# Kernel optimization log

Hardware: AMD Instinct MI355X
Metric: run time of the kernel (lower is better)

Reference implementation:

```python
import jax, jax.numpy as jnp
import numpy as np

B, L, D, H = 65536, 20, 4, 1024
T = 61  # output_length; 60 RK4 steps


def setup_inputs() -> dict:
    key = jax.random.key(0)
    ks = jax.random.split(key, 16)
    # small positive states so the quadratic SEIR dynamics stay finite over 60 steps
    xx = jax.random.uniform(ks[0], (B, L, D), dtype=jnp.float32) * 0.1
    dims = [L * D] + [H] * 6 + [3]
    inp = {"xx": xx}
    for i in range(7):
        scale = 1.0 / np.sqrt(dims[i])
        W = jax.random.normal(ks[1 + 2 * i], (dims[i], dims[i + 1]), dtype=jnp.float32) * scale
        if i == 6:
            W = W * 1e-3  # keep beta/gamma/sigma small -> stable integration
        inp[f"W{i}"] = W
        inp[f"b{i}"] = jnp.zeros((dims[i + 1],), jnp.float32)
    inp["output_length"] = T
    return inp


def reference(xx, W0, b0, W1, b1, W2, b2, W3, b3, W4, b4, W5, b5, W6, b6, output_length):
    h = xx.reshape(xx.shape[0], -1)  # (B, L*D)
    for W, b in ((W0, b0), (W1, b1), (W2, b2), (W3, b3), (W4, b4), (W5, b5)):
        h = jax.nn.leaky_relu(h @ W + b, negative_slope=0.01)
    out = h @ W6 + b6  # (B, 3)
    beta, gamma, sigma = out[:, 0:1], out[:, 1:2], out[:, 2:3]  # each (B,1)

    initial = xx[:, 0]  # (B, 4) = S,E,I,R at t0
    S0, E0, I0, R0 = (initial[:, i:i + 1] for i in range(4))
    # self.step = 1 in the torch module, so dt is folded in as 1.0

    def derivs(S, E, I):
        SI = beta * S * I
        return -SI, SI - sigma * E, sigma * E - gamma * I, gamma * I

    def body(carry, _):
        S, E, I, R = carry
        k1S, k1E, k1I, k1R = derivs(S, E, I)
        k2S, k2E, k2I, k2R = derivs(S + 0.5 * k1S, E + 0.5 * k1E, I + 0.5 * k1I)
        k3S, k3E, k3I, k3R = derivs(S + 0.5 * k2S, E + 0.5 * k2E, I + 0.5 * k2I)
        k4S, k4E, k4I, k4R = derivs(S + k3S, E + k3E, I + k3I)
        upd = lambda f, k1, k2, k3, k4: f + (k1 + 2 * k2 + 2 * k3 + k4) / 6.0
        new = (upd(S, k1S, k2S, k3S, k4S),
               upd(E, k1E, k2E, k3E, k4E),
               upd(I, k1I, k2I, k3I, k4I),
               upd(R, k1R, k2R, k3R, k4R))
        return new, jnp.concatenate(new, axis=1)  # (B,4) per step

    _, ys = jax.lax.scan(body, (S0, E0, I0, R0), None, length=output_length - 1)
    y0 = jnp.concatenate([S0, E0, I0, R0], axis=1)  # (B,4)
    y = jnp.concatenate([y0[None], ys], axis=0)     # (T,B,4)
    return jnp.transpose(y, (1, 0, 2))              # (B,T,4) in S,E,I,R order
```

## Files before the change

### kernel.cpp

```cpp
#include <hip/hip_runtime.h>
#include <stdint.h>

typedef short s16x8 __attribute__((ext_vector_type(8)));
typedef __bf16 bf16x8 __attribute__((ext_vector_type(8)));
typedef float f32x4 __attribute__((ext_vector_type(4)));

typedef const __attribute__((address_space(1))) void* gas_ptr;
typedef __attribute__((address_space(3))) void* las_ptr;

__device__ __forceinline__ unsigned short f2bf(float f) {
  unsigned u = __builtin_bit_cast(unsigned, f);
  u += 0x7FFFu + ((u >> 16) & 1u);
  return (unsigned short)(u >> 16);
}
__device__ __forceinline__ float bf2f(unsigned short h) {
  return __builtin_bit_cast(float, (unsigned)h << 16);
}
__device__ __forceinline__ void async16(const void* g, void* l) {
  __builtin_amdgcn_global_load_lds((gas_ptr)g, (las_ptr)l, 16, 0, 0);
}

__global__ void prep_x0(const float* __restrict__ xx, unsigned short* __restrict__ X0,
                        int rowOffset, int rows) {
  int idx = blockIdx.x * blockDim.x + threadIdx.x;
  if (idx >= rows * 128) return;
  int r = idx >> 7, c = idx & 127;
  float v = (c < 80) ? xx[(size_t)(rowOffset + r) * 80 + c] : 0.f;
  X0[(size_t)r * 128 + c] = f2bf(v);
}

struct TP {
  const float* W[6];
  unsigned short* WT[6];
};

__global__ void transpose_all(TP tp) {
  const int z = blockIdx.z;
  const int K  = (z == 0) ? 80  : 1024;
  const int KP = (z == 0) ? 128 : 1024;
  if (blockIdx.y * 32 >= KP) return;
  __shared__ float tile[32][33];
  const int n0 = blockIdx.x * 32, k0 = blockIdx.y * 32;
  const int tx = threadIdx.x, ty = threadIdx.y;
  const float* W = tp.W[z];
  unsigned short* WT = tp.WT[z];
  #pragma unroll
  for (int j = 0; j < 32; j += 8) {
    int k = k0 + ty + j;
    tile[ty + j][tx] = (k < K) ? W[(size_t)k * 1024 + n0 + tx] : 0.f;
  }
  __syncthreads();
  #pragma unroll
  for (int j = 0; j < 32; j += 8) {
    WT[(size_t)(n0 + ty + j) * KP + k0 + tx] = f2bf(tile[tx][ty + j]);
  }
}

#define BM 128
#define BN 128
#define BK 64

__global__ void gemm_mlp(const unsigned short* __restrict__ A,
                         const unsigned short* __restrict__ BT,
                         const float* __restrict__ bias,
                         unsigned short* __restrict__ C,
                         int M, int N, int K, int leaky) {
  __shared__ unsigned short As[BM * BK];
  __shared__ unsigned short Bs[BN * BK];

  const int tid  = threadIdx.x;
  const int wid  = tid >> 6;
  const int lane = tid & 63;
  const int wr = (wid >> 1) * 64;
  const int wc = (wid & 1) * 64;
  const int bn = blockIdx.x * BN;
  const int bm = blockIdx.y * BM;

  const int srow = lane >> 3;
  const int scol = (lane & 7) * 8;

  f32x4 acc[4][4] = {};

  const unsigned short* aTile = A  + (size_t)bm * K;
  const unsigned short* bTile = BT + (size_t)bn * K;

  for (int k0 = 0; k0 < K; k0 += BK) {
    #pragma unroll
    for (int j = 0; j < 4; ++j) {
      const int rg = wid + j * 4;
      async16(aTile + (size_t)(rg * 8 + srow) * K + k0 + scol, &As[rg * 8 * BK]);
      async16(bTile + (size_t)(rg * 8 + srow) * K + k0 + scol, &Bs[rg * 8 * BK]);
    }
    __syncthreads();

    const int fr = lane & 15;
    const int kq = (lane >> 4) * 8;
    #pragma unroll
    for (int ks = 0; ks < BK; ks += 32) {
      const int kk = ks + kq;
      bf16x8 af[4], bv[4];
      #pragma unroll
      for (int m = 0; m < 4; ++m)
        af[m] = __builtin_bit_cast(bf16x8, *(const s16x8*)&As[(wr + m * 16 + fr) * BK + kk]);
      #pragma unroll
      for (int n = 0; n < 4; ++n)
        bv[n] = __builtin_bit_cast(bf16x8, *(const s16x8*)&Bs[(wc + n * 16 + fr) * BK + kk]);
      #pragma unroll
      for (int m = 0; m < 4; ++m)
        #pragma unroll
        for (int n = 0; n < 4; ++n)
          acc[m][n] = __builtin_amdgcn_mfma_f32_16x16x32_bf16(af[m], bv[n], acc[m][n], 0, 0, 0);
    }
    __syncthreads();
  }

  const int fcol = lane & 15;
  const int frow = (lane >> 4) * 4;
  #pragma unroll
  for (int m = 0; m < 4; ++m) {
    #pragma unroll
    for (int n = 0; n < 4; ++n) {
      const int col = bn + wc + n * 16 + fcol;
      const float bb = bias[col];
      #pragma unroll
      for (int r = 0; r < 4; ++r) {
        const int row = bm + wr + m * 16 + frow + r;
        float v = acc[m][n][r] + bb;
        if (leaky) v = (v > 0.f) ? v : 0.01f * v;
        C[(size_t)row * N + col] = f2bf(v);
      }
    }
  }
}


__device__ __forceinline__ void stage_half(const char* srcRow0, size_t ldb,
                                           char* ldsHalf, int w, int rsub, int usw) {
  #pragma unroll
  for (int l = 0; l < 2; ++l) {
    const char* src = srcRow0 + (size_t)((l * 8 + w) * 8 + rsub) * ldb + usw;
    async16(src, ldsHalf + (l * 8 + w) * 1024);
  }
}

#define MFMA16 __builtin_amdgcn_mfma_f32_16x16x32_bf16
#define EPAD 72
#define EBYTES (64 * EPAD * 2)

template <int HEAD>
__global__ __launch_bounds__(512, 2)
void gemm8(const unsigned short* __restrict__ A,
           const unsigned short* __restrict__ BT,
           const float* __restrict__ bias,
           unsigned short* __restrict__ C,
           const float* __restrict__ W6,
           float* __restrict__ partial,
           int M, int N, int K) {
  extern __shared__ char smem[];
  char* smA = smem;
  char* smB = smem + 65536;
  const unsigned short* sA = (const unsigned short*)smA;
  const unsigned short* sB = (const unsigned short*)smB;
  const int NTk = K >> 6;

  const int tid  = threadIdx.x;
  const int w    = tid >> 6;
  const int lane = tid & 63;

  const int nwg = gridDim.x;
  const int bid = blockIdx.x;
  const int q = nwg >> 3, r = nwg & 7;
  const int xcd = bid & 7, idx = bid >> 3;
  const int wg = (xcd < r ? xcd * (q + 1) : r * (q + 1) + (xcd - r) * q) + idx;
  const int nNT = N >> 8;
  const int mtile = wg / nNT, ntile = wg % nNT;
  const int bm = mtile << 8, bn = ntile << 8;

  const int wr = (w >> 2) << 7;
  const int wc = (w & 3) << 6;
  const int fr = lane & 15;
  const int e0 = lane >> 4;
  const int sw = lane & 7;
  const int rsub = lane >> 3;
  const int usw  = ((sw ^ rsub) << 4);
  const int col0 = (((e0)     ^ sw) << 3);
  const int col1 = (((e0 + 4) ^ sw) << 3);

  const size_t ldb = (size_t)K * 2;
  const char* Ab = (const char*)A  + (size_t)bm * ldb;
  const char* Bb = (const char*)BT + (size_t)bn * ldb;

  f32x4 acc[8][4] = {};

#define RDA(c_, row_, col_) __builtin_bit_cast(bf16x8, *(const s16x8*)&sA[(c_) * 16384 + (row_) * 64 + (col_)])
#define RDB(c_, row_, col_) __builtin_bit_cast(bf16x8, *(const s16x8*)&sB[(c_) * 16384 + (row_) * 64 + (col_)])

  stage_half(Bb,                    ldb, smB,                  w, rsub, usw);
  stage_half(Bb + 128 * ldb,        ldb, smB + 16384,          w, rsub, usw);
  stage_half(Ab,                    ldb, smA,                  w, rsub, usw);
  stage_half(Ab + 128 * ldb,        ldb, smA + 16384,          w, rsub, usw);
  stage_half(Bb + 128,              ldb, smB + 32768,          w, rsub, usw);
  stage_half(Bb + 128 * ldb + 128,  ldb, smB + 32768 + 16384,  w, rsub, usw);
  asm volatile("s_waitcnt vmcnt(4)" ::: "memory");
  __builtin_amdgcn_s_barrier();

  for (int kt = 0; kt < NTk; ++kt) {
    const int c = kt & 1;
    bf16x8 aF[4][2], bF[4][2];

    #pragma unroll
    for (int m = 0; m < 4; ++m) {
      const int row = wr + m * 16 + fr;
      aF[m][0] = RDA(c, row, col0);
      aF[m][1] = RDA(c, row, col1);
    }
    #pragma unroll
    for (int n = 0; n < 2; ++n) {
      const int row = wc + n * 16 + fr;
      bF[n][0] = RDB(c, row, col0);
      bF[n][1] = RDB(c, row, col1);
    }
    if (kt + 1 < NTk)
      stage_half(Ab + (size_t)(kt + 1) * 128, ldb, smA + (c ^ 1) * 32768, w, rsub, usw);
    __builtin_amdgcn_s_barrier();
    __builtin_amdgcn_s_setprio(1);
    #pragma unroll
    for (int m = 0; m < 4; ++m)
      #pragma unroll
      for (int n = 0; n < 2; ++n) {
        acc[m][n] = MFMA16(aF[m][0], bF[n][0], acc[m][n], 0, 0, 0);
        acc[m][n] = MFMA16(aF[m][1], bF[n][1], acc[m][n], 0, 0, 0);
      }
    __builtin_amdgcn_s_setprio(0);
    __builtin_amdgcn_s_barrier();

    #pragma unroll
    for (int n = 2; n < 4; ++n) {
      const int row = wc + n * 16 + fr;
      bF[n][0] = RDB(c, row, col0);
      bF[n][1] = RDB(c, row, col1);
    }
    if (kt + 1 < NTk)
      stage_half(Ab + 128 * ldb + (size_t)(kt + 1) * 128, ldb,
                 smA + (c ^ 1) * 32768 + 16384, w, rsub, usw);
    __builtin_amdgcn_s_barrier();
    __builtin_amdgcn_s_setprio(1);
    #pragma unroll
    for (int m = 0; m < 4; ++m)
      #pragma unroll
      for (int n = 2; n < 4; ++n) {
        acc[m][n] = MFMA16(aF[m][0], bF[n][0], acc[m][n], 0, 0, 0);
        acc[m][n] = MFMA16(aF[m][1], bF[n][1], acc[m][n], 0, 0, 0);
      }
    __builtin_amdgcn_s_setprio(0);
    __builtin_amdgcn_s_barrier();

    #pragma unroll
    for (int m = 0; m < 4; ++m) {
      const int row = wr + (m + 4) * 16 + fr;
      aF[m][0] = RDA(c, row, col0);
      aF[m][1] = RDA(c, row, col1);
    }
    if (kt + 2 < NTk)
      stage_half(Bb + (size_t)(kt + 2) * 128, ldb, smB + c * 32768, w, rsub, usw);
    __builtin_amdgcn_s_barrier();
    __builtin_amdgcn_s_setprio(1);
    #pragma unroll
    for (int m = 0; m < 4; ++m)
      #pragma unroll
      for (int n = 0; n < 2; ++n) {
        acc[m + 4][n] = MFMA16(aF[m][0], bF[n][0], acc[m + 4][n], 0, 0, 0);
        acc[m + 4][n] = MFMA16(aF[m][1], bF[n][1], acc[m + 4][n], 0, 0, 0);
      }
    __builtin_amdgcn_s_setprio(0);
    __builtin_amdgcn_s_barrier();

    if (kt + 2 < NTk)
      stage_half(Bb + 128 * ldb + (size_t)(kt + 2) * 128, ldb,
                 smB + c * 32768 + 16384, w, rsub, usw);
    __builtin_amdgcn_s_barrier();
    __builtin_amdgcn_s_setprio(1);
    #pragma unroll
    for (int m = 0; m < 4; ++m)
      #pragma unroll
      for (int n = 2; n < 4; ++n) {
        acc[m + 4][n] = MFMA16(aF[m][0], bF[n][0], acc[m + 4][n], 0, 0, 0);
        acc[m + 4][n] = MFMA16(aF[m][1], bF[n][1], acc[m + 4][n], 0, 0, 0);
      }
    __builtin_amdgcn_s_setprio(0);
    if (kt + 2 < NTk) asm volatile("s_waitcnt vmcnt(4)" ::: "memory");
    else              asm volatile("s_waitcnt vmcnt(0)" ::: "memory");
    __builtin_amdgcn_s_barrier();
  }

#undef RDA
#undef RDB

  const int fcol = lane & 15;
  float bbv[4];
  #pragma unroll
  for (int n = 0; n < 4; ++n) bbv[n] = bias[bn + wc + n * 16 + fcol];

  if constexpr (HEAD) {
    float w6c[4][3];
    #pragma unroll
    for (int n = 0; n < 4; ++n) {
      const int col = bn + wc + n * 16 + fcol;
      #pragma unroll
      for (int j = 0; j < 3; ++j) w6c[n][j] = W6[col * 3 + j];
    }
    const int nt = bn >> 8;
    #pragma unroll
    for (int mh = 0; mh < 2; ++mh)
      #pragma unroll
      for (int mm = 0; mm < 4; ++mm)
        #pragma unroll
        for (int rr = 0; rr < 4; ++rr) {
          float s0 = 0.f, s1 = 0.f, s2 = 0.f;
          #pragma unroll
          for (int n = 0; n < 4; ++n) {
            float v = acc[mh * 4 + mm][n][rr] + bbv[n];
            v = (v > 0.f) ? v : 0.01f * v;
            s0 = fmaf(v, w6c[n][0], s0);
            s1 = fmaf(v, w6c[n][1], s1);
            s2 = fmaf(v, w6c[n][2], s2);
          }
          #pragma unroll
          for (int off = 1; off < 16; off <<= 1) {
            s0 += __shfl_xor(s0, off);
            s1 += __shfl_xor(s1, off);
            s2 += __shfl_xor(s2, off);
          }
          if (fcol == 0) {
            const int row = bm + wr + mh * 64 + mm * 16 + e0 * 4 + rr;
            *(float4*)&partial[((size_t)nt * M + row) * 4] =
                make_float4(s0, s1, s2, 0.f);
          }
        }
  } else {
    unsigned short* eb = (unsigned short*)(smem + w * EBYTES);
    const int r8 = lane >> 3, c8 = (lane & 7) * 8;
    #pragma unroll
    for (int mh = 0; mh < 2; ++mh) {
      #pragma unroll
      for (int mm = 0; mm < 4; ++mm)
        #pragma unroll
        for (int n = 0; n < 4; ++n)
          #pragma unroll
          for (int rr = 0; rr < 4; ++rr) {
            const int row64 = mm * 16 + e0 * 4 + rr;
            float v = acc[mh * 4 + mm][n][rr] + bbv[n];
            v = (v > 0.f) ? v : 0.01f * v;
            eb[row64 * EPAD + n * 16 + fcol] = f2bf(v);
          }
      asm volatile("" ::: "memory");
      #pragma unroll
      for (int rg = 0; rg < 8; ++rg) {
        const int row64 = rg * 8 + r8;
        s16x8 vv = *(const s16x8*)&eb[row64 * EPAD + c8];
        const int rl = bm + wr + mh * 64 + row64;
        *(s16x8*)&C[(size_t)rl * N + bn + wc + c8] = vv;
      }
      asm volatile("" ::: "memory");
    }
  }
}

__global__ void rk4_traj(const float* __restrict__ partial,
                         const float* __restrict__ b6,
                         const float* __restrict__ xx,
                         float* __restrict__ out,
                         int rowOffset, int rows, int T) {
  const int r = blockIdx.x * blockDim.x + threadIdx.x;
  if (r >= rows) return;
  const size_t grow = (size_t)rowOffset + r;

  float4 p0 = *(const float4*)&partial[((size_t)0 * rows + r) * 4];
  float4 p1 = *(const float4*)&partial[((size_t)1 * rows + r) * 4];
  float4 p2 = *(const float4*)&partial[((size_t)2 * rows + r) * 4];
  float4 p3 = *(const float4*)&partial[((size_t)3 * rows + r) * 4];
  const float beta  = p0.x + p1.x + p2.x + p3.x + b6[0];
  const float gamma = p0.y + p1.y + p2.y + p3.y + b6[1];
  const float sigma = p0.z + p1.z + p2.z + p3.z + b6[2];

  const float4 iv = *(const float4*)(xx + grow * 80);
  float S = iv.x, E = iv.y, I = iv.z, R = iv.w;
  float* o = out + grow * (size_t)T * 4;
  *(float4*)o = iv;

#define DERIVS(S_, E_, I_, dS, dE, dI, dR)      \
  {                                             \
    float SI = beta * (S_) * (I_);              \
    float sE = sigma * (E_);                    \
    float gI = gamma * (I_);                    \
    dS = -SI; dE = SI - sE; dI = sE - gI; dR = gI; \
  }

  for (int t = 1; t < T; ++t) {
    float k1S, k1E, k1I, k1R; DERIVS(S, E, I, k1S, k1E, k1I, k1R);
    float k2S, k2E, k2I, k2R; DERIVS(S + 0.5f * k1S, E + 0.5f * k1E, I + 0.5f * k1I, k2S, k2E, k2I, k2R);
    float k3S, k3E, k3I, k3R; DERIVS(S + 0.5f * k2S, E + 0.5f * k2E, I + 0.5f * k2I, k3S, k3E, k3I, k3R);
    float k4S, k4E, k4I, k4R; DERIVS(S + k3S, E + k3E, I + k3I, k4S, k4E, k4I, k4R);
    S += (k1S + 2.f * k2S + 2.f * k3S + k4S) * (1.f / 6.f);
    E += (k1E + 2.f * k2E + 2.f * k3E + k4E) * (1.f / 6.f);
    I += (k1I + 2.f * k2I + 2.f * k3I + k4I) * (1.f / 6.f);
    R += (k1R + 2.f * k2R + 2.f * k3R + k4R) * (1.f / 6.f);
    *(float4*)(o + (size_t)t * 4) = make_float4(S, E, I, R);
  }
#undef DERIVS
}

extern "C" void kernel_launch(void* const* d_in, const int* in_sizes, int n_in,
                              void* d_out, int out_size, void* d_ws, size_t ws_size,
                              hipStream_t stream) {
  const float* xx = (const float*)d_in[0];
  const float* W[7];
  const float* bb[7];
  for (int i = 0; i < 7; ++i) {
    W[i]  = (const float*)d_in[1 + 2 * i];
    bb[i] = (const float*)d_in[2 + 2 * i];
  }
  const int B = in_sizes[0] / 80;
  const int T = out_size / (B * 4);
  float* out = (float*)d_out;

  {
    auto k0 = gemm8<0>;
    auto k1 = gemm8<1>;
    hipFuncSetAttribute((const void*)k0, hipFuncAttributeMaxDynamicSharedMemorySize, 131072);
    hipFuncSetAttribute((const void*)k1, hipFuncAttributeMaxDynamicSharedMemorySize, 131072);
  }

  uint8_t* ws = (uint8_t*)d_ws;
  size_t off = 0;
  auto alloc = [&](size_t bytes) -> uint8_t* {
    uint8_t* p = ws + off;
    off += (bytes + 255) & ~(size_t)255;
    return p;
  };

  unsigned short* WTl[6];
  WTl[0] = (unsigned short*)alloc((size_t)1024 * 128 * 2);
  for (int i = 1; i < 6; ++i) WTl[i] = (unsigned short*)alloc((size_t)1024 * 1024 * 2);

  const size_t weightBytes = off;
  const size_t avail = ws_size > weightBytes ? ws_size - weightBytes : 0;
  int Bc = (int)(avail / 4416);
  Bc = (Bc / 256) * 256;
  if (Bc > B) Bc = B;
  if (Bc < 256) Bc = 256;

  unsigned short* X0   = (unsigned short*)alloc((size_t)Bc * 128 * 2);
  unsigned short* buf0 = (unsigned short*)alloc((size_t)Bc * 1024 * 2);
  unsigned short* buf1 = (unsigned short*)alloc((size_t)Bc * 1024 * 2);
  float* partial       = (float*)alloc((size_t)Bc * 4 * 16);

  {
    TP tp;
    for (int i = 0; i < 6; ++i) { tp.W[i] = W[i]; tp.WT[i] = WTl[i]; }
    transpose_all<<<dim3(32, 32, 6), dim3(32, 8), 0, stream>>>(tp);
  }

  for (int r0 = 0; r0 < B; r0 += Bc) {
    const int rows = (B - r0 < Bc) ? (B - r0) : Bc;

    {
      const int n = rows * 128;
      prep_x0<<<(n + 255) / 256, 256, 0, stream>>>(xx, X0, r0, rows);
    }

    gemm_mlp<<<dim3(8, rows / 128), 256, 0, stream>>>(X0, WTl[0], bb[0], buf0,
                                                      rows, 1024, 128, 1);

    const int nwg = (rows / 256) * 4;
    gemm8<0><<<nwg, 512, 131072, stream>>>(buf0, WTl[1], bb[1], buf1, nullptr, nullptr, rows, 1024, 1024);
    gemm8<0><<<nwg, 512, 131072, stream>>>(buf1, WTl[2], bb[2], buf0, nullptr, nullptr, rows, 1024, 1024);
    gemm8<0><<<nwg, 512, 131072, stream>>>(buf0, WTl[3], bb[3], buf1, nullptr, nullptr, rows, 1024, 1024);
    gemm8<0><<<nwg, 512, 131072, stream>>>(buf1, WTl[4], bb[4], buf0, nullptr, nullptr, rows, 1024, 1024);

    gemm8<1><<<nwg, 512, 131072, stream>>>(buf0, WTl[5], bb[5], nullptr, W[6], partial, rows, 1024, 1024);

    rk4_traj<<<(rows + 255) / 256, 256, 0, stream>>>(partial, bb[6], xx, out, r0, rows, T);
  }
}
```

Baseline: 959.9 us.

## Prefetch next k-tile A fragments across iterations and hoist W6 head loads

The GEMM main loop now reads the first half of the A fragments for the next k-tile from LDS inside the current iteration, once the global wait completes and before the last MFMA block, instead of at the top of the next iteration. This overlaps LDS read latency with MFMA work and removes a serial LDS-read phase at the start of each iteration. The head variant also loads its W6 column weights before the main loop so their global latency is hidden. The cost is more live VGPRs (aPre plus aF2, and the w6c values held through the loop), which could lower occupancy or cause spills.

```diff
diff --git a/kernel.cpp b/kernel.cpp
--- a/kernel.cpp
+++ b/kernel.cpp
@@ -185,10 +185,21 @@
   const int usw  = ((sw ^ rsub) << 4);
   const int col0 = (((e0)     ^ sw) << 3);
   const int col1 = (((e0 + 4) ^ sw) << 3);
+  const int fcol = lane & 15;
 
   const size_t ldb = (size_t)K * 2;
   const char* Ab = (const char*)A  + (size_t)bm * ldb;
   const char* Bb = (const char*)BT + (size_t)bn * ldb;
+
+  float w6c[4][3];
+  if constexpr (HEAD) {
+    #pragma unroll
+    for (int n = 0; n < 4; ++n) {
+      const int col = bn + wc + n * 16 + fcol;
+      #pragma unroll
+      for (int j = 0; j < 3; ++j) w6c[n][j] = W6[col * 3 + j];
+    }
+  }
 
   f32x4 acc[8][4] = {};
 
@@ -204,16 +215,18 @@
   asm volatile("s_waitcnt vmcnt(4)" ::: "memory");
   __builtin_amdgcn_s_barrier();
 
+  bf16x8 aPre[4][2];
+  #pragma unroll
+  for (int m = 0; m < 4; ++m) {
+    const int row = wr + m * 16 + fr;
+    aPre[m][0] = RDA(0, row, col0);
+    aPre[m][1] = RDA(0, row, col1);
+  }
+
   for (int kt = 0; kt < NTk; ++kt) {
     const int c = kt & 1;
-    bf16x8 aF[4][2], bF[4][2];
-
-    #pragma unroll
-    for (int m = 0; m < 4; ++m) {
-      const int row = wr + m * 16 + fr;
-      aF[m][0] = RDA(c, row, col0);
-      aF[m][1] = RDA(c, row, col1);
-    }
+    bf16x8 aF2[4][2], bF[4][2];
+
     #pragma unroll
     for (int n = 0; n < 2; ++n) {
       const int row = wc + n * 16 + fr;
@@ -228,8 +241,8 @@
     for (int m = 0; m < 4; ++m)
       #pragma unroll
       for (int n = 0; n < 2; ++n) {
-        acc[m][n] = MFMA16(aF[m][0], bF[n][0], acc[m][n], 0, 0, 0);
-        acc[m][n] = MFMA16(aF[m][1], bF[n][1], acc[m][n], 0, 0, 0);
+        acc[m][n] = MFMA16(aPre[m][0], bF[n][0], acc[m][n], 0, 0, 0);
+        acc[m][n] = MFMA16(aPre[m][1], bF[n][1], acc[m][n], 0, 0, 0);
       }
     __builtin_amdgcn_s_setprio(0);
     __builtin_amdgcn_s_barrier();
@@ -249,8 +262,8 @@
     for (int m = 0; m < 4; ++m)
       #pragma unroll
       for (int n = 2; n < 4; ++n) {
-        acc[m][n] = MFMA16(aF[m][0], bF[n][0], acc[m][n], 0, 0, 0);
-        acc[m][n] = MFMA16(aF[m][1], bF[n][1], acc[m][n], 0, 0, 0);
+        acc[m][n] = MFMA16(aPre[m][0], bF[n][0], acc[m][n], 0, 0, 0);
+        acc[m][n] = MFMA16(aPre[m][1], bF[n][1], acc[m][n], 0, 0, 0);
       }
     __builtin_amdgcn_s_setprio(0);
     __builtin_amdgcn_s_barrier();
@@ -258,8 +271,8 @@
     #pragma unroll
     for (int m = 0; m < 4; ++m) {
       const int row = wr + (m + 4) * 16 + fr;
-      aF[m][0] = RDA(c, row, col0);
-      aF[m][1] = RDA(c, row, col1);
+      aF2[m][0] = RDA(c, row, col0);
+      aF2[m][1] = RDA(c, row, col1);
     }
     if (kt + 2 < NTk)
       stage_half(Bb + (size_t)(kt + 2) * 128, ldb, smB + c * 32768, w, rsub, usw);
@@ -269,8 +282,8 @@
     for (int m = 0; m < 4; ++m)
       #pragma unroll
       for (int n = 0; n < 2; ++n) {
-        acc[m + 4][n] = MFMA16(aF[m][0], bF[n][0], acc[m + 4][n], 0, 0, 0);
-        acc[m + 4][n] = MFMA16(aF[m][1], bF[n][1], acc[m + 4][n], 0, 0, 0);
+        acc[m + 4][n] = MFMA16(aF2[m][0], bF[n][0], acc[m + 4][n], 0, 0, 0);
+        acc[m + 4][n] = MFMA16(aF2[m][1], bF[n][1], acc[m + 4][n], 0, 0, 0);
       }
     __builtin_amdgcn_s_setprio(0);
     __builtin_amdgcn_s_barrier();
@@ -278,37 +291,37 @@
     if (kt + 2 < NTk)
       stage_half(Bb + 128 * ldb + (size_t)(kt + 2) * 128, ldb,
                  smB + c * 32768 + 16384, w, rsub, usw);
-    __builtin_amdgcn_s_barrier();
-    __builtin_amdgcn_s_setprio(1);
-    #pragma unroll
-    for (int m = 0; m < 4; ++m)
-      #pragma unroll
-      for (int n = 2; n < 4; ++n) {
-        acc[m + 4][n] = MFMA16(aF[m][0], bF[n][0], acc[m + 4][n], 0, 0, 0);
-        acc[m + 4][n] = MFMA16(aF[m][1], bF[n][1], acc[m + 4][n], 0, 0, 0);
-      }
-    __builtin_amdgcn_s_setprio(0);
     if (kt + 2 < NTk) asm volatile("s_waitcnt vmcnt(4)" ::: "memory");
     else              asm volatile("s_waitcnt vmcnt(0)" ::: "memory");
+    if (kt + 1 < NTk) {
+      #pragma unroll
+      for (int m = 0; m < 4; ++m) {
+        const int row = wr + m * 16 + fr;
+        aPre[m][0] = RDA(c ^ 1, row, col0);
+        aPre[m][1] = RDA(c ^ 1, row, col1);
+      }
+    }
+    __builtin_amdgcn_s_barrier();
+    __builtin_amdgcn_s_setprio(1);
+    #pragma unroll
+    for (int m = 0; m < 4; ++m)
+      #pragma unroll
+      for (int n = 2; n < 4; ++n) {
+        acc[m + 4][n] = MFMA16(aF2[m][0], bF[n][0], acc[m + 4][n], 0, 0, 0);
+        acc[m + 4][n] = MFMA16(aF2[m][1], bF[n][1], acc[m + 4][n], 0, 0, 0);
+      }
+    __builtin_amdgcn_s_setprio(0);
     __builtin_amdgcn_s_barrier();
   }
 
 #undef RDA
 #undef RDB
 
-  const int fcol = lane & 15;
   float bbv[4];
   #pragma unroll
   for (int n = 0; n < 4; ++n) bbv[n] = bias[bn + wc + n * 16 + fcol];
 
   if constexpr (HEAD) {
-    float w6c[4][3];
-    #pragma unroll
-    for (int n = 0; n < 4; ++n) {
-      const int col = bn + wc + n * 16 + fcol;
-      #pragma unroll
-      for (int j = 0; j < 3; ++j) w6c[n][j] = W6[col * 3 + j];
-    }
     const int nt = bn >> 8;
     #pragma unroll
     for (int mh = 0; mh < 2; ++mh)
```

Result: no change. 972.9 us (+1.4%).
